# Optimization experiments

Hardware: AMD Instinct MI355X
Metric: run time of the kernel (lower is better)

## Reference

```python
import jax, jax.numpy as jnp
import numpy as np

N_NODES = 100000
N_EDGES = 3200000
IN_CH, HID, OUT_CH = 128, 16, 64


def setup_inputs() -> dict:
    key = jax.random.key(0)
    k1, k2, k3, k4 = jax.random.split(key, 4)
    x = jax.random.normal(k1, (N_NODES, IN_CH), dtype=jnp.float32)
    edge_index = jax.random.randint(k2, (2, N_EDGES), 0, N_NODES, dtype=jnp.int64)
    # Glorot-ish init for weights, zeros for bias (PyG GCNConv default)
    W1 = jax.random.normal(k3, (IN_CH, HID), dtype=jnp.float32) / np.sqrt(IN_CH)
    b1 = jnp.zeros((HID,), dtype=jnp.float32)
    W2 = jax.random.normal(k4, (HID, OUT_CH), dtype=jnp.float32) / np.sqrt(HID)
    b2 = jnp.zeros((OUT_CH,), dtype=jnp.float32)
    return {"x": x, "edge_index": edge_index, "W1": W1, "b1": b1, "W2": W2, "b2": b2}


def _gcn_conv(x, src, dst, W, b, n_nodes):
    """PyG GCNConv: linear -> symmetric-norm gather/scatter -> +bias.
    src/dst already include self-loops."""
    h = x @ W  # [N, F_out]
    deg = jax.ops.segment_sum(jnp.ones_like(dst, dtype=h.dtype), dst,
                              num_segments=n_nodes)  # in-degree incl. self-loop
    deg_inv_sqrt = jnp.where(deg > 0, jax.lax.rsqrt(deg), 0.0)
    norm = deg_inv_sqrt[src] * deg_inv_sqrt[dst]  # [E+N]
    msg = h[src] * norm[:, None]  # gather + scale
    out = jax.ops.segment_sum(msg, dst, num_segments=n_nodes)  # scatter-add
    return out + b


def reference(x, edge_index, W1, b1, W2, b2):
    n_nodes = x.shape[0]
    loop = jnp.arange(n_nodes, dtype=edge_index.dtype)
    src = jnp.concatenate([edge_index[0], loop])  # add self-loops
    dst = jnp.concatenate([edge_index[1], loop])
    h = _gcn_conv(x, src, dst, W1, b1, n_nodes)
    h = jax.nn.relu(h)
    out = _gcn_conv(h, src, dst, W2, b2, n_nodes)
    return out
```

## Files before the change

### kernel.cpp

```cpp
#include <hip/hip_runtime.h>
#include <hip/hip_fp16.h>

constexpr int N      = 100000;
constexpr int E      = 3200000;
constexpr int IN_CH  = 128;
constexpr int HID    = 16;
constexpr int OUT_CH = 64;

constexpr int NPB    = 128;
constexpr int NB     = (N + NPB - 1) / NPB;
constexpr int PBLK   = 256;
constexpr int CHUNK  = E / PBLK;
static_assert(E % PBLK == 0, "uniform chunks");
constexpr int PTHR   = 1024;
constexpr int NITER  = (CHUNK + PTHR - 1) / PTHR;
constexpr unsigned CAP = 6144;
constexpr unsigned SENT = (unsigned)N;

typedef float nfloat4 __attribute__((ext_vector_type(4)));

__global__ __launch_bounds__(1024) void k_partition(const int* __restrict__ ei,
                                                    unsigned* __restrict__ bcnt,
                                                    unsigned* __restrict__ packed) {
    __shared__ unsigned staged[CHUNK];
    __shared__ unsigned short sb[CHUNK];
    __shared__ unsigned cnt[NB];
    __shared__ unsigned cur[NB];
    __shared__ unsigned goff[NB];
    __shared__ unsigned s[PTHR];

    int k = blockIdx.x, t = threadIdx.x;
    for (int b = t; b < NB; b += PTHR) cnt[b] = 0;
    __syncthreads();

    int e0 = k * CHUNK;
    unsigned vq[NITER];
    unsigned short bq[NITER];
    #pragma unroll
    for (int i = 0; i < NITER; ++i) {
        int idx = t + i * PTHR;
        if (i < NITER - 1 || idx < CHUNK) {
            int e = e0 + idx;
            unsigned sv = (unsigned)__builtin_nontemporal_load(ei + e);
            unsigned d  = (unsigned)__builtin_nontemporal_load(ei + E + e);
            unsigned b  = d >> 7;
            vq[i] = ((d & 127u) << 17) | sv;
            bq[i] = (unsigned short)b;
            atomicAdd(&cnt[b], 1u);
        }
    }
    __syncthreads();

    unsigned own = (t < NB) ? cnt[t] : 0u;
    s[t] = own;
    __syncthreads();
    for (int off = 1; off < PTHR; off <<= 1) {
        unsigned u = (t >= off) ? s[t - off] : 0u;
        __syncthreads();
        s[t] += u;
        __syncthreads();
    }
    if (t < NB) {
        unsigned ex = s[t] - own;
        cur[t] = ex;
        unsigned start = own ? atomicAdd(&bcnt[t], own) : 0u;
        goff[t] = t * CAP + start - ex;
    }
    __syncthreads();

    #pragma unroll
    for (int i = 0; i < NITER; ++i) {
        int idx = t + i * PTHR;
        if (i < NITER - 1 || idx < CHUNK) {
            unsigned b = bq[i];
            unsigned slot = atomicAdd(&cur[b], 1u);
            staged[slot] = vq[i];
            sb[slot] = (unsigned short)b;
        }
    }
    __syncthreads();

    for (int i = t; i < CHUNK; i += PTHR) {
        unsigned b = sb[i];
        unsigned pos = goff[b] + i;
        if (pos < (b + 1u) * CAP) packed[pos] = staged[i];
    }
}

__global__ __launch_bounds__(512) void k_sort(const unsigned* __restrict__ packed,
                                              const unsigned* __restrict__ bcnt,
                                              unsigned* __restrict__ sorted,
                                              uint2* __restrict__ ns2,
                                              float* __restrict__ dinv) {
    __shared__ unsigned stage[CAP];
    __shared__ unsigned outb[CAP];
    __shared__ unsigned cnt[NPB];
    __shared__ unsigned pp[NPB];
    __shared__ unsigned cur[NPB];
    __shared__ unsigned cpad_s;
    int b = blockIdx.x, t = threadIdx.x;
    if (t < NPB) cnt[t] = 0;
    unsigned e0 = (unsigned)b * CAP;
    unsigned c  = min(bcnt[b], CAP);
    __syncthreads();
    for (unsigned i = t; i < c; i += 512) {
        unsigned p = __builtin_nontemporal_load(packed + e0 + i);
        stage[i] = p;
        atomicAdd(&cnt[p >> 17], 1u);
    }
    __syncthreads();
    unsigned pcnt = 0;
    if (t < NPB) {
        pcnt = (cnt[t] + 15u) & ~15u;
        pp[t] = pcnt;
    }
    __syncthreads();
    for (int off = 1; off < NPB; off <<= 1) {
        unsigned u = (t < NPB && t >= off) ? pp[t - off] : 0u;
        __syncthreads();
        if (t < NPB) pp[t] += u;
        __syncthreads();
    }
    if (t < NPB) {
        unsigned ex = pp[t] - pcnt;
        cur[t] = ex;
        int node = b * NPB + t;
        if (node < N) {
            uint2 seg;
            seg.x = e0 + ex;
            seg.y = e0 + min(pp[t], CAP);
            ns2[node] = seg;
            dinv[node] = rsqrtf((float)cnt[t] + 1.0f);
        }
        if (t == NPB - 1) cpad_s = min(pp[t], CAP);
    }
    __syncthreads();
    unsigned cpad = cpad_s;
    for (unsigned i = t; i < cpad; i += 512) outb[i] = SENT;
    __syncthreads();
    for (unsigned i = t; i < c; i += 512) {
        unsigned p = stage[i];
        unsigned slot = atomicAdd(&cur[p >> 17], 1u);
        if (slot < CAP) outb[slot] = p & 0x1FFFFu;
    }
    __syncthreads();
    for (unsigned i = t; i < cpad; i += 512)
        __builtin_nontemporal_store(outb[i], sorted + e0 + i);
}

__global__ __launch_bounds__(256) void k_lin1(const float* __restrict__ x,
                                              const float* __restrict__ W1,
                                              const float* __restrict__ dinv,
                                              __half* __restrict__ h1s) {
    __shared__ float W1T[HID][IN_CH + 4];
    __shared__ float xs[16][IN_CH + 4];
    int t = threadIdx.x;
    for (int i = t; i < IN_CH * HID; i += 256) {
        int k = i >> 4, c = i & 15;
        W1T[c][k] = W1[i];
    }
    int rb = blockIdx.x * 16;
    const float4* xblk = (const float4*)(x + (size_t)rb * IN_CH);
    for (int i4 = t; i4 < 16 * IN_CH / 4; i4 += 256) {
        int r = i4 >> 5, c4 = i4 & 31;
        *(float4*)&xs[r][c4 * 4] = xblk[i4];
    }
    __syncthreads();

    int r = t >> 4, c = t & 15;
    int row = rb + r;
    const float4* xr = (const float4*)xs[r];
    const float4* wr = (const float4*)W1T[c];
    float acc = 0.f;
    #pragma unroll
    for (int k4 = 0; k4 < IN_CH / 4; ++k4) {
        float4 a = xr[k4], w = wr[k4];
        acc += a.x * w.x + a.y * w.y + a.z * w.z + a.w * w.w;
    }
    __half hv = __float2half_rn(dinv[row] * acc);
    __builtin_nontemporal_store(*(const unsigned short*)&hv,
                                (unsigned short*)(h1s + (size_t)row * HID + c));
}

__device__ __forceinline__ void accum8(float* acc, const float4& raw) {
    const __half2* hp = (const __half2*)&raw;
    #pragma unroll
    for (int j = 0; j < 4; ++j) {
        float2 f = __half22float2(hp[j]);
        acc[2 * j] += f.x;
        acc[2 * j + 1] += f.y;
    }
}


__global__ __launch_bounds__(256) void k_agg1(const unsigned* __restrict__ sorted,
                                              const uint2* __restrict__ ns2,
                                              const float* __restrict__ dinv,
                                              const __half* __restrict__ h1s,
                                              const float* __restrict__ b1,
                                              __half* __restrict__ h2s) {
    int t = threadIdx.x;
    int wave = (blockIdx.x << 2) + (t >> 6);
    int lane = t & 63;
    int nw = lane >> 3, slot = lane & 7;
    int eslot = slot >> 1, half = slot & 1;
    int wid = (wave << 3) + nw;
    uint2 seg = ns2[wid];
    unsigned s0 = seg.x, s1 = seg.y;
    float di = dinv[wid];
    float4 bb = *(const float4*)(b1 + half * 8);
    float4 bb2 = *(const float4*)(b1 + half * 8 + 4);
    float4 selfraw = *(const float4*)(h1s + (size_t)wid * HID + half * 8);

    float acc[8];
    {
        const __half2* hp = (const __half2*)&selfraw;
        float m = (eslot == 0) ? 1.f : 0.f;
        #pragma unroll
        for (int j = 0; j < 4; ++j) {
            float2 f = __half22float2(hp[j]);
            acc[2 * j] = m * f.x;
            acc[2 * j + 1] = m * f.y;
        }
    }
    for (unsigned e = s0 + (eslot << 2); e < s1; e += 16) {
        unsigned idx[4];
        float4 g[4];
        #pragma unroll
        for (int j = 0; j < 4; ++j)
            idx[j] = __builtin_nontemporal_load(sorted + e + j);
        #pragma unroll
        for (int j = 0; j < 4; ++j)
            g[j] = *(const float4*)(h1s + (size_t)idx[j] * HID + half * 8);
        #pragma unroll
        for (int j = 0; j < 4; ++j) accum8(acc, g[j]);
    }
    #pragma unroll
    for (int j = 0; j < 8; ++j) acc[j] += __shfl_xor(acc[j], 2, 64);
    #pragma unroll
    for (int j = 0; j < 8; ++j) acc[j] += __shfl_xor(acc[j], 4, 64);

    if (eslot == 0) {
        float bv[8] = {bb.x, bb.y, bb.z, bb.w, bb2.x, bb2.y, bb2.z, bb2.w};
        __half2 tmp[4];
        #pragma unroll
        for (int j = 0; j < 4; ++j) {
            float o0 = di * fmaxf(di * acc[2 * j] + bv[2 * j], 0.f);
            float o1 = di * fmaxf(di * acc[2 * j + 1] + bv[2 * j + 1], 0.f);
            tmp[j] = __float22half2_rn(float2{o0, o1});
        }
        nfloat4 ow = *(const nfloat4*)tmp;
        __builtin_nontemporal_store(ow, (nfloat4*)(h2s + (size_t)wid * HID + half * 8));
    }
}

__global__ __launch_bounds__(256) void k_agg2(const unsigned* __restrict__ sorted,
                                              const uint2* __restrict__ ns2,
                                              const float* __restrict__ dinv,
                                              const __half* __restrict__ h2s,
                                              const float* __restrict__ W2,
                                              const float* __restrict__ b2,
                                              float* __restrict__ out) {
    __shared__ float W2s[HID * OUT_CH];
    __shared__ float as[32][HID];
    int t = threadIdx.x;
    for (int i = t; i < HID * OUT_CH; i += 256) W2s[i] = W2[i];

    int wave = t >> 6;
    int lane = t & 63;
    int nw = lane >> 3, slot = lane & 7;
    int eslot = slot >> 1, half = slot & 1;
    int wnode = (wave << 3) + nw;
    int wid = (blockIdx.x << 5) + wnode;
    uint2 seg = ns2[wid];
    unsigned s0 = seg.x, s1 = seg.y;
    float di = dinv[wid];
    float4 selfraw = *(const float4*)(h2s + (size_t)wid * HID + half * 8);

    float acc[8];
    {
        const __half2* hp = (const __half2*)&selfraw;
        float m = (eslot == 0) ? 1.f : 0.f;
        #pragma unroll
        for (int j = 0; j < 4; ++j) {
            float2 f = __half22float2(hp[j]);
            acc[2 * j] = m * f.x;
            acc[2 * j + 1] = m * f.y;
        }
    }
    for (unsigned e = s0 + (eslot << 2); e < s1; e += 16) {
        unsigned idx[4];
        float4 g[4];
        #pragma unroll
        for (int j = 0; j < 4; ++j)
            idx[j] = __builtin_nontemporal_load(sorted + e + j);
        #pragma unroll
        for (int j = 0; j < 4; ++j)
            g[j] = *(const float4*)(h2s + (size_t)idx[j] * HID + half * 8);
        #pragma unroll
        for (int j = 0; j < 4; ++j) accum8(acc, g[j]);
    }
    #pragma unroll
    for (int j = 0; j < 8; ++j) acc[j] += __shfl_xor(acc[j], 2, 64);
    #pragma unroll
    for (int j = 0; j < 8; ++j) acc[j] += __shfl_xor(acc[j], 4, 64);

    if (eslot == 0) {
        #pragma unroll
        for (int j = 0; j < 8; ++j) as[wnode][half * 8 + j] = di * acc[j];
    }
    __syncthreads();

    int node = t >> 3;
    int c8 = (t & 7) * 8;
    float o[8];
    *(float4*)&o[0] = *(const float4*)&b2[c8];
    *(float4*)&o[4] = *(const float4*)&b2[c8 + 4];
    #pragma unroll
    for (int k = 0; k < HID; ++k) {
        float a = as[node][k];
        const float* w = &W2s[k * OUT_CH + c8];
        #pragma unroll
        for (int j = 0; j < 8; ++j) o[j] += a * w[j];
    }
    float* op = out + ((size_t)(blockIdx.x << 5) + node) * OUT_CH + c8;
    __builtin_nontemporal_store(nfloat4{o[0], o[1], o[2], o[3]}, (nfloat4*)op);
    __builtin_nontemporal_store(nfloat4{o[4], o[5], o[6], o[7]}, (nfloat4*)(op + 4));
}

extern "C" void kernel_launch(void* const* d_in, const int* in_sizes, int n_in,
                              void* d_out, int out_size, void* d_ws, size_t ws_size,
                              hipStream_t stream) {
    const float* x  = (const float*)d_in[0];
    const int*   ei = (const int*)d_in[1];
    const float* W1 = (const float*)d_in[2];
    const float* b1 = (const float*)d_in[3];
    const float* W2 = (const float*)d_in[4];
    const float* b2 = (const float*)d_in[5];
    float* out = (float*)d_out;

    char* ws = (char*)d_ws;
    float*    dinv   = (float*)(ws);
    uint2*    ns2    = (uint2*)(ws + 524288);
    unsigned* bcnt   = (unsigned*)(ws + 1441792);
    __half*   h1s    = (__half*)(ws + 2097152);
    __half*   h2s    = (__half*)(ws + 5505024);
    unsigned* packed = (unsigned*)(ws + 9437184);
    unsigned* sorted = (unsigned*)(ws + 29360128);

    hipMemsetAsync(bcnt, 0, NB * sizeof(unsigned), stream);
    hipMemsetAsync(h1s + (size_t)N * HID, 0, HID * sizeof(__half), stream);
    hipMemsetAsync(h2s + (size_t)N * HID, 0, HID * sizeof(__half), stream);
    k_partition <<<PBLK, PTHR, 0, stream>>>(ei, bcnt, packed);
    k_sort      <<<NB, 512, 0, stream>>>(packed, bcnt, sorted, ns2, dinv);
    k_lin1      <<<N / 16, 256, 0, stream>>>(x, W1, dinv, h1s);
    k_agg1      <<<N / 32, 256, 0, stream>>>(sorted, ns2, dinv, h1s, b1, h2s);
    k_agg2      <<<N / 32, 256, 0, stream>>>(sorted, ns2, dinv, h2s, W2, b2, out);
}
```

Before: 129.0 us.

## Vectorize index loads, drop nontemporal stores, fold sentinel memsets into lin1

```diff
diff --git a/kernel.cpp b/kernel.cpp
--- a/kernel.cpp
+++ b/kernel.cpp
@@ -17,7 +17,8 @@
 constexpr unsigned CAP = 6144;
 constexpr unsigned SENT = (unsigned)N;
 
-typedef float nfloat4 __attribute__((ext_vector_type(4)));
+typedef float    nfloat4 __attribute__((ext_vector_type(4)));
+typedef unsigned nuint4  __attribute__((ext_vector_type(4)));
 
 __global__ __launch_bounds__(1024) void k_partition(const int* __restrict__ ei,
                                                     unsigned* __restrict__ bcnt,
@@ -145,16 +146,22 @@
     }
     __syncthreads();
     for (unsigned i = t; i < cpad; i += 512)
-        __builtin_nontemporal_store(outb[i], sorted + e0 + i);
+        sorted[e0 + i] = outb[i];
 }
 
 __global__ __launch_bounds__(256) void k_lin1(const float* __restrict__ x,
                                               const float* __restrict__ W1,
                                               const float* __restrict__ dinv,
-                                              __half* __restrict__ h1s) {
+                                              __half* __restrict__ h1s,
+                                              __half* __restrict__ h2s) {
     __shared__ float W1T[HID][IN_CH + 4];
     __shared__ float xs[16][IN_CH + 4];
     int t = threadIdx.x;
+    if (blockIdx.x == 0 && t < 2 * HID) {
+        __half* dst = (t < HID) ? (h1s + (size_t)N * HID + t)
+                                : (h2s + (size_t)N * HID + (t - HID));
+        *dst = __float2half_rn(0.f);
+    }
     for (int i = t; i < IN_CH * HID; i += 256) {
         int k = i >> 4, c = i & 15;
         W1T[c][k] = W1[i];
@@ -177,9 +184,7 @@
         float4 a = xr[k4], w = wr[k4];
         acc += a.x * w.x + a.y * w.y + a.z * w.z + a.w * w.w;
     }
-    __half hv = __float2half_rn(dinv[row] * acc);
-    __builtin_nontemporal_store(*(const unsigned short*)&hv,
-                                (unsigned short*)(h1s + (size_t)row * HID + c));
+    h1s[(size_t)row * HID + c] = __float2half_rn(dinv[row] * acc);
 }
 
 __device__ __forceinline__ void accum8(float* acc, const float4& raw) {
@@ -224,14 +229,11 @@
         }
     }
     for (unsigned e = s0 + (eslot << 2); e < s1; e += 16) {
-        unsigned idx[4];
+        nuint4 iv = __builtin_nontemporal_load((const nuint4*)(sorted + e));
         float4 g[4];
         #pragma unroll
         for (int j = 0; j < 4; ++j)
-            idx[j] = __builtin_nontemporal_load(sorted + e + j);
-        #pragma unroll
-        for (int j = 0; j < 4; ++j)
-            g[j] = *(const float4*)(h1s + (size_t)idx[j] * HID + half * 8);
+            g[j] = *(const float4*)(h1s + (size_t)iv[j] * HID + half * 8);
         #pragma unroll
         for (int j = 0; j < 4; ++j) accum8(acc, g[j]);
     }
@@ -249,8 +251,7 @@
             float o1 = di * fmaxf(di * acc[2 * j + 1] + bv[2 * j + 1], 0.f);
             tmp[j] = __float22half2_rn(float2{o0, o1});
         }
-        nfloat4 ow = *(const nfloat4*)tmp;
-        __builtin_nontemporal_store(ow, (nfloat4*)(h2s + (size_t)wid * HID + half * 8));
+        *(float4*)(h2s + (size_t)wid * HID + half * 8) = *(const float4*)tmp;
     }
 }
 
@@ -289,14 +290,11 @@
         }
     }
     for (unsigned e = s0 + (eslot << 2); e < s1; e += 16) {
-        unsigned idx[4];
+        nuint4 iv = __builtin_nontemporal_load((const nuint4*)(sorted + e));
         float4 g[4];
         #pragma unroll
         for (int j = 0; j < 4; ++j)
-            idx[j] = __builtin_nontemporal_load(sorted + e + j);
-        #pragma unroll
-        for (int j = 0; j < 4; ++j)
-            g[j] = *(const float4*)(h2s + (size_t)idx[j] * HID + half * 8);
+            g[j] = *(const float4*)(h2s + (size_t)iv[j] * HID + half * 8);
         #pragma unroll
         for (int j = 0; j < 4; ++j) accum8(acc, g[j]);
     }
@@ -349,11 +347,9 @@
     unsigned* sorted = (unsigned*)(ws + 29360128);
 
     hipMemsetAsync(bcnt, 0, NB * sizeof(unsigned), stream);
-    hipMemsetAsync(h1s + (size_t)N * HID, 0, HID * sizeof(__half), stream);
-    hipMemsetAsync(h2s + (size_t)N * HID, 0, HID * sizeof(__half), stream);
     k_partition <<<PBLK, PTHR, 0, stream>>>(ei, bcnt, packed);
     k_sort      <<<NB, 512, 0, stream>>>(packed, bcnt, sorted, ns2, dinv);
-    k_lin1      <<<N / 16, 256, 0, stream>>>(x, W1, dinv, h1s);
+    k_lin1      <<<N / 16, 256, 0, stream>>>(x, W1, dinv, h1s, h2s);
     k_agg1      <<<N / 32, 256, 0, stream>>>(sorted, ns2, dinv, h1s, b1, h2s);
     k_agg2      <<<N / 32, 256, 0, stream>>>(sorted, ns2, dinv, h2s, W2, b2, out);
 }
```

Result: faster. 124.8 us (-3.2%).
